# Kernel optimization log

Hardware: AMD Instinct MI355X
Metric: run time of the kernel (lower is better)

## Reference

```python
import jax, jax.numpy as jnp
import numpy as np

NUM_RBF = 16; TOP_K = 32; EDGE_F = 128; NODE_F = 128; NUM_POS = 16; MAX_REL = 32
B, L, M = 2, 1024, 25
# atom order: N=0, Ca=1, C=2, O=3, Cb=4; 24 pairs after the (Ca,Ca) D_neighbors term,
# in the exact order of the torch forward's RBF_all list
PAIR_A = jnp.array([0,2,3,4,1,1,1,1,0,0,0,4,4,3,0,2,3,4,2,3,4,2,3,2])
PAIR_B = jnp.array([0,2,3,4,0,2,3,4,2,3,4,2,3,2,1,1,1,1,0,0,0,4,4,3])


def _rbf(D):
    mu = jnp.linspace(2.0, 22.0, NUM_RBF)
    sig = (22.0 - 2.0) / NUM_RBF
    return jnp.exp(-((D[..., None] - mu) / sig) ** 2)


def _ln(x, g, b, eps=1e-5):
    m = x.mean(-1, keepdims=True)
    v = ((x - m) ** 2).mean(-1, keepdims=True)
    return (x - m) * jax.lax.rsqrt(v + eps) * g + b


def _normalize(v):
    n = jnp.linalg.norm(v, axis=-1, keepdims=True)
    return v / jnp.maximum(n, 1e-12)


def setup_inputs():
    key = jax.random.key(0)
    ks = jax.random.split(key, 16)
    def w(i, shape, scale):
        return jax.random.normal(ks[i], shape, jnp.float32) * scale
    ar = jnp.arange(120, dtype=jnp.int32)
    return {
        "X": w(0, (B, L, 4, 3), 3.0),
        "Y": w(1, (B, L, M, 3), 3.0),
        "Y_m": jnp.ones((B, L, M), jnp.float32),
        "Y_t": jax.random.randint(ks[2], (B, L, M), 0, 120, jnp.int32),
        "mask": jnp.ones((B, L), jnp.float32),
        "R_idx": jnp.tile(jnp.arange(L, dtype=jnp.int32), (B, 1)),
        "chain_labels": jnp.zeros((B, L), jnp.int32),
        # learned params; torch Linear y = x @ W.T + b stored here as [in,out]
        "pos_W": w(3, (2 * MAX_REL + 2, NUM_POS), 0.1),
        "pos_b": jnp.zeros((NUM_POS,), jnp.float32),
        "edge_W": w(4, (NUM_POS + 25 * NUM_RBF, EDGE_F), 0.05),
        "ln_e_g": jnp.ones((EDGE_F,), jnp.float32), "ln_e_b": jnp.zeros((EDGE_F,), jnp.float32),
        "npd_W": w(5, (5 * NUM_RBF + 64 + 4, NODE_F), 0.08),
        "npd_b": jnp.zeros((NODE_F,), jnp.float32),
        "ln_n_g": jnp.ones((NODE_F,), jnp.float32), "ln_n_b": jnp.zeros((NODE_F,), jnp.float32),
        "type_W": w(6, (147, 64), 0.08), "type_b": jnp.zeros((64,), jnp.float32),
        "yn_W": w(7, (147, NODE_F), 0.08),
        "ye_W": w(8, (NUM_RBF, NODE_F), 0.2),
        "ln_ye_g": jnp.ones((NODE_F,), jnp.float32), "ln_ye_b": jnp.zeros((NODE_F,), jnp.float32),
        "ln_yn_g": jnp.ones((NODE_F,), jnp.float32), "ln_yn_b": jnp.zeros((NODE_F,), jnp.float32),
        # periodic table: [atomic_number, group(<19), period(<8)] per element id
        "ptable": jnp.stack([ar, ar % 19, ar % 8]),
    }


def reference(X, Y, Y_m, Y_t, mask, R_idx, chain_labels, pos_W, pos_b, edge_W,
              ln_e_g, ln_e_b, npd_W, npd_b, ln_n_g, ln_n_b, type_W, type_b,
              yn_W, ye_W, ln_ye_g, ln_ye_b, ln_yn_g, ln_yn_b, ptable):
    N, Ca, C, O = X[:, :, 0], X[:, :, 1], X[:, :, 2], X[:, :, 3]
    b = Ca - N; c = C - Ca
    a = jnp.cross(b, c)
    Cb = -0.58273431 * a + 0.56802827 * b - 0.54067466 * c + Ca

    # masked Ca-Ca distances + kNN (smallest)
    m2 = mask[:, :, None] * mask[:, None, :]
    D = m2 * jnp.sqrt(((Ca[:, :, None, :] - Ca[:, None, :, :]) ** 2).sum(-1) + 1e-6)
    D_adjust = D + (1.0 - m2) * D.max(-1, keepdims=True)
    k = min(TOP_K, L)
    neg_D, E_idx = jax.lax.top_k(-D_adjust, k)
    D_neighbors = -neg_D  # [B,L,k]

    atoms = jnp.stack([N, Ca, C, O, Cb])  # [5,B,L,3]
    def pair_rbf(ai, bi):
        A = atoms[ai]; Bc = atoms[bi]
        Dab = jnp.sqrt(((A[:, :, None, :] - Bc[:, None, :, :]) ** 2).sum(-1) + 1e-6)
        return _rbf(jnp.take_along_axis(Dab, E_idx, axis=2))  # [B,L,k,16]
    rbf_pairs = jax.vmap(pair_rbf)(PAIR_A, PAIR_B)  # [24,B,L,k,16]
    RBF_all = jnp.concatenate([_rbf(D_neighbors)[:, :, :, None, :],
                               jnp.moveaxis(rbf_pairs, 0, 3)], axis=3)
    RBF_all = RBF_all.reshape(RBF_all.shape[0], RBF_all.shape[1], k, 25 * NUM_RBF)

    # positional encodings over gathered neighbor offsets
    offset = jnp.take_along_axis(R_idx[:, :, None] - R_idx[:, None, :], E_idx, axis=2)
    d_chains = (chain_labels[:, :, None] == chain_labels[:, None, :]).astype(jnp.int32)
    E_chains = jnp.take_along_axis(d_chains, E_idx, axis=2)
    d = jnp.clip(offset + MAX_REL, 0, 2 * MAX_REL) * E_chains + (1 - E_chains) * (2 * MAX_REL + 1)
    E_pos = jax.nn.one_hot(d, 2 * MAX_REL + 2, dtype=jnp.float32) @ pos_W + pos_b

    E = jnp.concatenate([E_pos, RBF_all], -1) @ edge_W
    E = _ln(E, ln_e_g, ln_e_b)

    # ligand atom type features
    Y_t_1hot_ = jnp.concatenate([
        jax.nn.one_hot(Y_t, 120, dtype=jnp.float32),
        jax.nn.one_hot(ptable[1][Y_t], 19, dtype=jnp.float32),
        jax.nn.one_hot(ptable[2][Y_t], 8, dtype=jnp.float32)], -1)  # [B,L,M,147]
    Y_t_1hot = Y_t_1hot_ @ type_W + type_b  # [B,L,M,64]

    def rbf_to_Y(A):
        return _rbf(jnp.sqrt(((A[:, :, None, :] - Y) ** 2).sum(-1) + 1e-6))
    D_Y = jnp.concatenate([rbf_to_Y(A) for A in (N, Ca, C, O, Cb)], -1)  # [B,L,M,80]

    # local-frame angle features (A=N, B=Ca, C=C)
    e1 = _normalize(N - Ca)
    v2 = C - Ca
    e2 = _normalize(v2 - e1 * (e1 * v2).sum(-1, keepdims=True))
    e3 = jnp.cross(e1, e2)
    R_res = jnp.stack([e1, e2, e3], axis=-1)  # [B,L,3,3], columns e1,e2,e3
    local = jnp.einsum('blqp,blyq->blyp', R_res, Y - Ca[:, :, None, :])
    rxy = jnp.sqrt(local[..., 0] ** 2 + local[..., 1] ** 2 + 1e-8)
    rxyz = jnp.linalg.norm(local, axis=-1) + 1e-8
    f_angles = jnp.stack([local[..., 0] / rxy, local[..., 1] / rxy,
                          rxy / rxyz, local[..., 2] / rxyz], -1)  # [B,L,M,4]

    V = jnp.concatenate([D_Y, Y_t_1hot, f_angles], -1) @ npd_W + npd_b
    V = _ln(V, ln_n_g, ln_n_b)

    Y_edges = _rbf(jnp.sqrt(((Y[:, :, :, None, :] - Y[:, :, None, :, :]) ** 2).sum(-1) + 1e-6)) @ ye_W
    Y_edges = _ln(Y_edges, ln_ye_g, ln_ye_b)
    Y_nodes = _ln(Y_t_1hot_ @ yn_W, ln_yn_g, ln_yn_b)
    return V, E, E_idx, Y_nodes, Y_edges, Y_m
```

## Files before the change

kernel.cpp:

```cpp
#include <hip/hip_runtime.h>
#include <hip/hip_bf16.h>
#include <stdint.h>

#define BB 2
#define LLEN 1024
#define MM 25
#define KK 32

#define OFF_V   0
#define OFF_E   6553600
#define OFF_EI  14942208
#define OFF_YN  15007744
#define OFF_YE  21561344
#define OFF_YM  185401344

#define KP 424
#define KP2 168
#define NR 5

#define NB_YE  (BB*LLEN)
#define NB_E   (BB*LLEN/2)
#define NB_N   ((BB*LLEN+NR-1)/NR)
#define NB_YN  (BB*LLEN*MM/4)
#define VB_E   NB_YE
#define VB_N   (VB_E + NB_E)
#define VB_YN  (VB_N + NB_N)
#define VB_END (VB_YN + NB_YN)

#define SCRATCH_BYTES (680*1024)

typedef __attribute__((ext_vector_type(8))) short short8_t;
typedef __attribute__((ext_vector_type(4))) float f32x4;

__constant__ int g_PA[24] = {0,2,3,4,1,1,1,1,0,0,0,4,4,3,0,2,3,4,2,3,4,2,3,2};
__constant__ int g_PB[24] = {0,2,3,4,0,2,3,4,2,3,4,2,3,2,1,1,1,1,0,0,0,4,4,3};

__device__ __forceinline__ float rbf_val(float d, int r) {
    float mu = 2.0f + (20.0f / 15.0f) * (float)r;
    float z = (d - mu) * 0.8f;
    return __expf(-z * z);
}

__global__ __launch_bounds__(256) void k_pretopk(
    const float* __restrict__ X, const float* __restrict__ mask,
    const float* __restrict__ W, const float* __restrict__ yeW,
    const float* __restrict__ npdW,
    __hip_bfloat16* __restrict__ Bp, __hip_bfloat16* __restrict__ Bp2,
    __hip_bfloat16* __restrict__ Bp3,
    int* __restrict__ eidx, float* __restrict__ dnb,
    float* __restrict__ outEI)
{
    __shared__ float sx[1024], syy[1024], sz[1024], sm[1024];
    int tid = threadIdx.x;

    if (blockIdx.x >= 512) {
        int idx = (blockIdx.x - 512) * 256 + tid;
        if (idx < 6656) {
            int lane = idx & 63, tt = (idx >> 6) & 7, ks = idx >> 9;
            int k0 = ks*32 + (lane >> 4)*8;
            int n  = tt*16 + (lane & 15);
            __hip_bfloat16* dst = Bp + (size_t)idx * 8;
            #pragma unroll
            for (int j = 0; j < 8; ++j) dst[j] = __float2bfloat16(W[(size_t)(k0 + j)*128 + n]);
        } else if (idx < 7168) {
            int i2 = idx - 6656;
            int lane = i2 & 63, tt = i2 >> 6;
            int kg = lane >> 4;
            int n  = tt*16 + (lane & 15);
            __hip_bfloat16* dst = Bp2 + (size_t)i2 * 8;
            #pragma unroll
            for (int j = 0; j < 8; ++j) {
                float v = (kg < 2) ? yeW[(size_t)(kg*8 + j)*128 + n] : 0.0f;
                dst[j] = __float2bfloat16(v);
            }
        } else if (idx < 9728) {
            int i3 = idx - 7168;
            int lane = i3 & 63, tt = (i3 >> 6) & 7, ks = i3 >> 9;
            int k0 = ks*32 + (lane >> 4)*8;
            int n  = tt*16 + (lane & 15);
            __hip_bfloat16* dst = Bp3 + (size_t)i3 * 8;
            #pragma unroll
            for (int j = 0; j < 8; ++j) {
                int k = k0 + j;
                float v = (k < 148) ? npdW[(size_t)k*128 + n] : 0.0f;
                dst[j] = __float2bfloat16(v);
            }
        }
        return;
    }

    int wid = tid >> 6, lane = tid & 63;
    int row0 = blockIdx.x * 4;
    int b = row0 >> 10;
    const float* Xb = X + (size_t)b * LLEN * 12;
    const float* mb = mask + b * LLEN;
    for (int j = tid; j < 1024; j += 256) {
        sx[j]  = Xb[j*12+3];
        syy[j] = Xb[j*12+4];
        sz[j]  = Xb[j*12+5];
        sm[j]  = mb[j];
    }
    __syncthreads();

    int row = row0 + wid, i = row & 1023;
    float cax = sx[i], cay = syy[i], caz = sz[i];
    float mi = sm[i];

    float df[16], mm_[16];
    float lmax = 0.0f;
    #pragma unroll
    for (int q = 0; q < 16; ++q) {
        int j = q*64 + lane;
        float dx = cax - sx[j];
        float dy = cay - syy[j];
        float dz = caz - sz[j];
        float m2 = mi * sm[j];
        float d = sqrtf(dx*dx + dy*dy + dz*dz + 1e-6f) * m2;
        df[q] = d; mm_[q] = m2;
        lmax = fmaxf(lmax, d);
    }
    #pragma unroll
    for (int o = 32; o > 0; o >>= 1) lmax = fmaxf(lmax, __shfl_xor(lmax, o));

    unsigned long long pack[16];
    #pragma unroll
    for (int q = 0; q < 16; ++q) {
        float da = df[q] + (1.0f - mm_[q]) * lmax;
        pack[q] = ((unsigned long long)__float_as_uint(da) << 32) | (unsigned)(q*64 + lane);
    }

    int   myJw = 0;
    float myDv = 0.0f;
    for (int it = 0; it < KK; ++it) {
        unsigned long long lmin = pack[0];
        #pragma unroll
        for (int q = 1; q < 16; ++q) if (pack[q] < lmin) lmin = pack[q];
        #pragma unroll
        for (int o = 32; o > 0; o >>= 1) {
            unsigned long long other = __shfl_xor(lmin, o);
            if (other < lmin) lmin = other;
        }
        int jw = (int)(lmin & 0xffffffffu);
        if (lane == it) { myJw = jw; myDv = __uint_as_float((unsigned)(lmin >> 32)); }
        int lw = jw & 63, qw = jw >> 6;
        #pragma unroll
        for (int q = 0; q < 16; ++q)
            if (lane == lw && q == qw) pack[q] = ~0ull;
    }
    if (lane < KK) {
        eidx[row*KK + lane]  = myJw;
        dnb [row*KK + lane]  = myDv;
        outEI[row*KK + lane] = (float)myJw;
    }
}

union SMem {
    struct { __hip_bfloat16 A[64*KP]; float aj[64][16]; float ai[2][16]; int didx[64]; } e;
    struct { __hip_bfloat16 A[128*KP2]; float sat[NR][15]; float sfr[NR][9]; } n;
    struct { float sy4[32][4]; float stage[4][16*132]; } y;
};

__global__ __launch_bounds__(256) void k_main(
    int vbase,
    const float* __restrict__ X, const float* __restrict__ Y,
    const int* __restrict__ Ridx, const int* __restrict__ chain,
    const float* __restrict__ posW, const float* __restrict__ posb,
    const __hip_bfloat16* __restrict__ Bpack,
    const float* __restrict__ lnEg, const float* __restrict__ lnEb,
    const int* __restrict__ eidx, const float* __restrict__ dnb,
    const int* __restrict__ Yt,
    const float* __restrict__ typeW, const float* __restrict__ typeb,
    const int* __restrict__ ptab,
    const __hip_bfloat16* __restrict__ Bpack3, const float* __restrict__ npdb,
    const float* __restrict__ lnNg, const float* __restrict__ lnNb,
    const __hip_bfloat16* __restrict__ Bpack2,
    const float* __restrict__ lnYEg, const float* __restrict__ lnYEb,
    const float* __restrict__ Ym, const float* __restrict__ ynW,
    const float* __restrict__ lnYNg, const float* __restrict__ lnYNb,
    float* __restrict__ outV, float* __restrict__ outE,
    float* __restrict__ outYN, float* __restrict__ outYE,
    float* __restrict__ outYM)
{
    __shared__ __align__(16) SMem sm;
    int vb = blockIdx.x + vbase;
    int tid = threadIdx.x;
    int wv = tid >> 6, lane = tid & 63;
    int col16 = lane & 15, kg = lane >> 4;

    if (vb >= VB_YN) {
        int row = (vb - VB_YN) * 4 + wv;
        int t = Yt[row];
        int p1 = ptab[120 + t], p2 = ptab[240 + t];
        int r0 = t, r1 = 120 + p1, r2 = 139 + p2;
        float x0 = ynW[r0*128 + lane] + ynW[r1*128 + lane] + ynW[r2*128 + lane];
        float x1 = ynW[r0*128 + 64 + lane] + ynW[r1*128 + 64 + lane] + ynW[r2*128 + 64 + lane];
        float s = x0 + x1, s2 = x0*x0 + x1*x1;
        #pragma unroll
        for (int o = 1; o < 64; o <<= 1) { s += __shfl_xor(s, o); s2 += __shfl_xor(s2, o); }
        float mean = s * (1.0f/128.0f);
        float var  = s2 * (1.0f/128.0f) - mean*mean;
        float inv  = rsqrtf(var + 1e-5f);
        size_t base = (size_t)row * 128;
        outYN[base + lane]      = (x0 - mean)*inv*lnYNg[lane]    + lnYNb[lane];
        outYN[base + 64 + lane] = (x1 - mean)*inv*lnYNg[64+lane] + lnYNb[64+lane];
        if (lane == 0) outYM[row] = Ym[row];
        return;
    }

    if (vb < NB_YE) {
        int row = vb;
        if (tid < 32) { sm.y.sy4[tid][0]=0.f; sm.y.sy4[tid][1]=0.f; sm.y.sy4[tid][2]=0.f; sm.y.sy4[tid][3]=0.f; }
        __syncthreads();
        if (tid < MM*3) ((float*)sm.y.sy4)[ (tid/3)*4 + (tid%3) ] = Y[(size_t)row * MM * 3 + tid];

        short8_t bfr[8];
        const short8_t* B2 = (const short8_t*)Bpack2;
        #pragma unroll
        for (int t = 0; t < 8; ++t) bfr[t] = B2[t*64 + lane];
        float g[8], be[8];
        #pragma unroll
        for (int t = 0; t < 8; ++t) { g[t] = lnYEg[t*16 + col16]; be[t] = lnYEb[t*16 + col16]; }
        __syncthreads();

        float* outR = outYE + (size_t)row * 625 * 128;
        float* sbuf = sm.y.stage[wv];
        for (int T = wv; T < 40; T += 4) {
            int p0 = T * 16;
            int p  = p0 + col16;
            int pc = p < 624 ? p : 624;
            int m1 = pc / 25, m2 = pc - 25*m1;
            float dx = sm.y.sy4[m1][0] - sm.y.sy4[m2][0];
            float dy = sm.y.sy4[m1][1] - sm.y.sy4[m2][1];
            float dz = sm.y.sy4[m1][2] - sm.y.sy4[m2][2];
            float d = sqrtf(dx*dx + dy*dy + dz*dz + 1e-6f);
            union { short8_t v; __hip_bfloat16 h[8]; } ua;
            if (kg < 2) {
                #pragma unroll
                for (int j = 0; j < 8; ++j) ua.h[j] = __float2bfloat16(rbf_val(d, kg*8 + j));
            } else {
                ua.v = (short8_t){0,0,0,0,0,0,0,0};
            }
            f32x4 acc[8];
            #pragma unroll
            for (int t = 0; t < 8; ++t)
                acc[t] = __builtin_amdgcn_mfma_f32_16x16x32_bf16(ua.v, bfr[t],
                             (f32x4){0.f,0.f,0.f,0.f}, 0, 0, 0);
            #pragma unroll
            for (int r = 0; r < 4; ++r) {
                float s = 0.0f;
                #pragma unroll
                for (int t = 0; t < 8; ++t) s += acc[t][r];
                s += __shfl_xor(s, 1); s += __shfl_xor(s, 2);
                s += __shfl_xor(s, 4); s += __shfl_xor(s, 8);
                float mean = s * (1.0f/128.0f);
                float q2 = 0.0f;
                #pragma unroll
                for (int t = 0; t < 8; ++t) { float c0 = acc[t][r] - mean; q2 += c0*c0; }
                q2 += __shfl_xor(q2, 1); q2 += __shfl_xor(q2, 2);
                q2 += __shfl_xor(q2, 4); q2 += __shfl_xor(q2, 8);
                float inv = rsqrtf(q2 * (1.0f/128.0f) + 1e-5f);
                float* sr = sbuf + (kg*4 + r) * 132;
                #pragma unroll
                for (int t = 0; t < 8; ++t) sr[t*16 + col16] = (acc[t][r] - mean)*inv*g[t] + be[t];
            }
            #pragma unroll
            for (int it = 0; it < 8; ++it) {
                int off = it*256 + lane*4;
                int rr = (off >> 7), cc = off & 127;
                float4 v = *(const float4*)(sbuf + rr*132 + cc);
                int gbase = p0*128 + off;
                if (gbase < 80000) *(float4*)(outR + gbase) = v;
            }
        }
        return;
    }

    if (vb < VB_N) {
        int r0 = (vb - VB_E) * 2;
        int b  = r0 >> 10;
        const float* Xb = X + (size_t)b * LLEN * 12;

        if (tid < 64) {
            int e = tid, row = r0 + (e >> 5), k = e & 31;
            int j = eidx[row*KK + k];
            const float* xr = Xb + j*12;
            float nx=xr[0], ny=xr[1], nz=xr[2];
            float ax=xr[3], ay=xr[4], az=xr[5];
            float cx=xr[6], cy=xr[7], cz=xr[8];
            float bx=ax-nx, by=ay-ny, bz=az-nz;
            float vx=cx-ax, vy=cy-ay, vz=cz-az;
            float qx = by*vz - bz*vy, qy = bz*vx - bx*vz, qz = bx*vy - by*vx;
            sm.e.aj[e][0]=nx; sm.e.aj[e][1]=ny; sm.e.aj[e][2]=nz;
            sm.e.aj[e][3]=ax; sm.e.aj[e][4]=ay; sm.e.aj[e][5]=az;
            sm.e.aj[e][6]=cx; sm.e.aj[e][7]=cy; sm.e.aj[e][8]=cz;
            sm.e.aj[e][9]=xr[9]; sm.e.aj[e][10]=xr[10]; sm.e.aj[e][11]=xr[11];
            sm.e.aj[e][12] = -0.58273431f*qx + 0.56802827f*bx - 0.54067466f*vx + ax;
            sm.e.aj[e][13] = -0.58273431f*qy + 0.56802827f*by - 0.54067466f*vy + ay;
            sm.e.aj[e][14] = -0.58273431f*qz + 0.56802827f*bz - 0.54067466f*vz + az;
            int off = Ridx[row] - Ridx[b*LLEN + j];
            int ec = (chain[row] == chain[b*LLEN + j]) ? 1 : 0;
            int dc = off + 32; dc = dc < 0 ? 0 : (dc > 64 ? 64 : dc);
            sm.e.didx[e] = ec ? dc : 65;
        }
        if (tid >= 64 && tid < 66) {
            int rl = tid - 64;
            int i = (r0 + rl) & 1023;
            const float* xr = Xb + i*12;
            float nx=xr[0], ny=xr[1], nz=xr[2];
            float ax=xr[3], ay=xr[4], az=xr[5];
            float cx=xr[6], cy=xr[7], cz=xr[8];
            float bx=ax-nx, by=ay-ny, bz=az-nz;
            float vx=cx-ax, vy=cy-ay, vz=cz-az;
            float qx = by*vz - bz*vy, qy = bz*vx - bx*vz, qz = bx*vy - by*vx;
            sm.e.ai[rl][0]=nx; sm.e.ai[rl][1]=ny; sm.e.ai[rl][2]=nz;
            sm.e.ai[rl][3]=ax; sm.e.ai[rl][4]=ay; sm.e.ai[rl][5]=az;
            sm.e.ai[rl][6]=cx; sm.e.ai[rl][7]=cy; sm.e.ai[rl][8]=cz;
            sm.e.ai[rl][9]=xr[9]; sm.e.ai[rl][10]=xr[10]; sm.e.ai[rl][11]=xr[11];
            sm.e.ai[rl][12] = -0.58273431f*qx + 0.56802827f*bx - 0.54067466f*vx + ax;
            sm.e.ai[rl][13] = -0.58273431f*qy + 0.56802827f*by - 0.54067466f*vy + ay;
            sm.e.ai[rl][14] = -0.58273431f*qz + 0.56802827f*bz - 0.54067466f*vz + az;
        }
        __syncthreads();

        for (int item = tid; item < 64 * 26; item += 256) {
            int e = item / 26, it = item - e * 26;
            int rl = e >> 5;
            union { short8_t v[2]; __hip_bfloat16 h[16]; } uf;
            if (it == 0) {
                int d = sm.e.didx[e];
                #pragma unroll
                for (int c = 0; c < 16; ++c) uf.h[c] = __float2bfloat16(posW[d*16 + c] + posb[c]);
            } else {
                float dist;
                if (it == 1) {
                    dist = dnb[(r0 + rl)*KK + (e & 31)];
                } else {
                    int p = it - 2;
                    int a = g_PA[p], q = g_PB[p];
                    float dx = sm.e.ai[rl][a*3+0] - sm.e.aj[e][q*3+0];
                    float dy = sm.e.ai[rl][a*3+1] - sm.e.aj[e][q*3+1];
                    float dz = sm.e.ai[rl][a*3+2] - sm.e.aj[e][q*3+2];
                    dist = sqrtf(dx*dx + dy*dy + dz*dz + 1e-6f);
                }
                #pragma unroll
                for (int r = 0; r < 16; ++r) uf.h[r] = __float2bfloat16(rbf_val(dist, r));
            }
            short8_t* dst = (short8_t*)(sm.e.A + e * KP + it * 16);
            dst[0] = uf.v[0];
            dst[1] = uf.v[1];
        }
        __syncthreads();

        int wid = tid >> 6;
        f32x4 acc[8];
        #pragma unroll
        for (int t = 0; t < 8; ++t) acc[t] = (f32x4){0.f, 0.f, 0.f, 0.f};
        const __hip_bfloat16* Ar = sm.e.A + (wid*16 + col16) * KP + kg * 8;
        const short8_t* Bp = (const short8_t*)Bpack;
        for (int ks = 0; ks < 13; ++ks) {
            short8_t a = *(const short8_t*)(Ar + ks*32);
            #pragma unroll
            for (int t = 0; t < 8; ++t) {
                short8_t bf = Bp[(ks*8 + t)*64 + lane];
                acc[t] = __builtin_amdgcn_mfma_f32_16x16x32_bf16(a, bf, acc[t], 0, 0, 0);
            }
        }
        __syncthreads();

        float* sbuf = (float*)sm.e.A + wid * (16*132);
        float g[8], be[8];
        #pragma unroll
        for (int t = 0; t < 8; ++t) { g[t] = lnEg[t*16 + col16]; be[t] = lnEb[t*16 + col16]; }
        #pragma unroll
        for (int r = 0; r < 4; ++r) {
            float s = 0.0f;
            #pragma unroll
            for (int t = 0; t < 8; ++t) s += acc[t][r];
            s += __shfl_xor(s, 1); s += __shfl_xor(s, 2);
            s += __shfl_xor(s, 4); s += __shfl_xor(s, 8);
            float mean = s * (1.0f/128.0f);
            float q2 = 0.0f;
            #pragma unroll
            for (int t = 0; t < 8; ++t) { float c0 = acc[t][r] - mean; q2 += c0*c0; }
            q2 += __shfl_xor(q2, 1); q2 += __shfl_xor(q2, 2);
            q2 += __shfl_xor(q2, 4); q2 += __shfl_xor(q2, 8);
            float inv = rsqrtf(q2 * (1.0f/128.0f) + 1e-5f);
            float* sr = sbuf + (kg*4 + r) * 132;
            #pragma unroll
            for (int t = 0; t < 8; ++t) sr[t*16 + col16] = (acc[t][r] - mean)*inv*g[t] + be[t];
        }
        float* gdst = outE + ((size_t)r0 * KK + wid*16) * 128;
        #pragma unroll
        for (int it = 0; it < 8; ++it) {
            int off = it*256 + lane*4;
            int rr = off >> 7, cc = off & 127;
            float4 v = *(const float4*)(sbuf + rr*132 + cc);
            *(float4*)(gdst + off) = v;
        }
        return;
    }

    {
        int r0 = (vb - VB_N) * NR;
        int nrows = (2048 - r0) < NR ? (2048 - r0) : NR;
        int natoms = nrows * MM;

        if (tid < nrows) {
            int row = r0 + tid;
            int b = row >> 10, i = row & 1023;
            const float* xr = X + ((size_t)b * LLEN + i) * 12;
            float nx=xr[0], ny=xr[1], nz=xr[2];
            float ax=xr[3], ay=xr[4], az=xr[5];
            float cx=xr[6], cy=xr[7], cz=xr[8];
            float bx=ax-nx, by=ay-ny, bz=az-nz;
            float vx=cx-ax, vy=cy-ay, vz=cz-az;
            float qx = by*vz - bz*vy, qy = bz*vx - bx*vz, qz = bx*vy - by*vx;
            sm.n.sat[tid][0]=nx; sm.n.sat[tid][1]=ny; sm.n.sat[tid][2]=nz;
            sm.n.sat[tid][3]=ax; sm.n.sat[tid][4]=ay; sm.n.sat[tid][5]=az;
            sm.n.sat[tid][6]=cx; sm.n.sat[tid][7]=cy; sm.n.sat[tid][8]=cz;
            sm.n.sat[tid][9]=xr[9]; sm.n.sat[tid][10]=xr[10]; sm.n.sat[tid][11]=xr[11];
            sm.n.sat[tid][12] = -0.58273431f*qx + 0.56802827f*bx - 0.54067466f*vx + ax;
            sm.n.sat[tid][13] = -0.58273431f*qy + 0.56802827f*by - 0.54067466f*vy + ay;
            sm.n.sat[tid][14] = -0.58273431f*qz + 0.56802827f*bz - 0.54067466f*vz + az;
            float e1x = nx-ax, e1y = ny-ay, e1z = nz-az;
            float n1 = fmaxf(sqrtf(e1x*e1x+e1y*e1y+e1z*e1z), 1e-12f);
            e1x/=n1; e1y/=n1; e1z/=n1;
            float dd = e1x*vx + e1y*vy + e1z*vz;
            float u2x = vx - e1x*dd, u2y = vy - e1y*dd, u2z = vz - e1z*dd;
            float n2 = fmaxf(sqrtf(u2x*u2x+u2y*u2y+u2z*u2z), 1e-12f);
            u2x/=n2; u2y/=n2; u2z/=n2;
            sm.n.sfr[tid][0]=e1x; sm.n.sfr[tid][1]=e1y; sm.n.sfr[tid][2]=e1z;
            sm.n.sfr[tid][3]=u2x; sm.n.sfr[tid][4]=u2y; sm.n.sfr[tid][5]=u2z;
            sm.n.sfr[tid][6]=e1y*u2z - e1z*u2y;
            sm.n.sfr[tid][7]=e1z*u2x - e1x*u2z;
            sm.n.sfr[tid][8]=e1x*u2y - e1y*u2x;
        }
        __syncthreads();

        for (int item = tid; item < natoms * 10; item += 256) {
            int a = item / 10, it = item - a * 10;
            int rl = a / MM, m = a - rl * MM;
            int row = r0 + rl;
            const float* Yb = Y + (size_t)row * MM * 3 + m * 3;
            union { short8_t v[2]; __hip_bfloat16 h[16]; } uf;
            if (it < 5) {
                float dx = sm.n.sat[rl][it*3+0] - Yb[0];
                float dy = sm.n.sat[rl][it*3+1] - Yb[1];
                float dz = sm.n.sat[rl][it*3+2] - Yb[2];
                float dist = sqrtf(dx*dx + dy*dy + dz*dz + 1e-6f);
                #pragma unroll
                for (int r = 0; r < 16; ++r) uf.h[r] = __float2bfloat16(rbf_val(dist, r));
            } else if (it < 9) {
                int qq = it - 5;
                int t = Yt[row*MM + m];
                int p1 = ptab[120 + t], p2 = ptab[240 + t];
                #pragma unroll
                for (int c = 0; c < 16; ++c) {
                    int cc = qq*16 + c;
                    uf.h[c] = __float2bfloat16(typeW[t*64 + cc] + typeW[(120+p1)*64 + cc]
                            + typeW[(139+p2)*64 + cc] + typeb[cc]);
                }
            } else {
                float vx = Yb[0] - sm.n.sat[rl][3];
                float vy = Yb[1] - sm.n.sat[rl][4];
                float vz = Yb[2] - sm.n.sat[rl][5];
                float l0 = sm.n.sfr[rl][0]*vx + sm.n.sfr[rl][1]*vy + sm.n.sfr[rl][2]*vz;
                float l1 = sm.n.sfr[rl][3]*vx + sm.n.sfr[rl][4]*vy + sm.n.sfr[rl][5]*vz;
                float l2 = sm.n.sfr[rl][6]*vx + sm.n.sfr[rl][7]*vy + sm.n.sfr[rl][8]*vz;
                float rxy  = sqrtf(l0*l0 + l1*l1 + 1e-8f);
                float rxyz = sqrtf(l0*l0 + l1*l1 + l2*l2) + 1e-8f;
                uf.h[0] = __float2bfloat16(l0 / rxy);
                uf.h[1] = __float2bfloat16(l1 / rxy);
                uf.h[2] = __float2bfloat16(rxy / rxyz);
                uf.h[3] = __float2bfloat16(l2 / rxyz);
                #pragma unroll
                for (int c = 4; c < 16; ++c) uf.h[c] = __float2bfloat16(0.0f);
            }
            short8_t* dst = (short8_t*)(sm.n.A + a * KP2 + it * 16);
            dst[0] = uf.v[0];
            dst[1] = uf.v[1];
        }
        __syncthreads();

        int wid = tid >> 6;
        const short8_t* Bp = (const short8_t*)Bpack3;
        float g[8], be[8], bias[8];
        #pragma unroll
        for (int t = 0; t < 8; ++t) {
            g[t] = lnNg[t*16 + col16]; be[t] = lnNb[t*16 + col16];
            bias[t] = npdb[t*16 + col16];
        }
        #pragma unroll
        for (int half = 0; half < 2; ++half) {
            int tile = wid + half*4;
            int abase = tile * 16;
            if (abase < natoms) {
                const __hip_bfloat16* Ar = sm.n.A + (abase + col16) * KP2 + kg * 8;
                f32x4 acc[8];
                #pragma unroll
                for (int t = 0; t < 8; ++t) acc[t] = (f32x4){0.f, 0.f, 0.f, 0.f};
                for (int ks = 0; ks < 5; ++ks) {
                    short8_t a = *(const short8_t*)(Ar + ks*32);
                    #pragma unroll
                    for (int t = 0; t < 8; ++t) {
                        short8_t bf = Bp[(ks*8 + t)*64 + lane];
                        acc[t] = __builtin_amdgcn_mfma_f32_16x16x32_bf16(a, bf, acc[t], 0, 0, 0);
                    }
                }
                #pragma unroll
                for (int r = 0; r < 4; ++r) {
                    float s = 0.0f;
                    #pragma unroll
                    for (int t = 0; t < 8; ++t) { acc[t][r] += bias[t]; s += acc[t][r]; }
                    s += __shfl_xor(s, 1); s += __shfl_xor(s, 2);
                    s += __shfl_xor(s, 4); s += __shfl_xor(s, 8);
                    float mean = s * (1.0f/128.0f);
                    float q2 = 0.0f;
                    #pragma unroll
                    for (int t = 0; t < 8; ++t) { float c0 = acc[t][r] - mean; q2 += c0*c0; }
                    q2 += __shfl_xor(q2, 1); q2 += __shfl_xor(q2, 2);
                    q2 += __shfl_xor(q2, 4); q2 += __shfl_xor(q2, 8);
                    float inv = rsqrtf(q2 * (1.0f/128.0f) + 1e-5f);
                    int aa = abase + kg*4 + r;
                    if (aa < natoms) {
                        float* dst = outV + ((size_t)r0 * MM + aa) * 128 + col16;
                        #pragma unroll
                        for (int t = 0; t < 8; ++t) dst[t*16] = (acc[t][r] - mean)*inv*g[t] + be[t];
                    }
                }
            }
        }
    }
}

extern "C" void kernel_launch(void* const* d_in, const int* in_sizes, int n_in,
                              void* d_out, int out_size, void* d_ws, size_t ws_size,
                              hipStream_t stream) {
    const float* X     = (const float*)d_in[0];
    const float* Y     = (const float*)d_in[1];
    const float* Ym    = (const float*)d_in[2];
    const int*   Yt    = (const int*)d_in[3];
    const float* mask  = (const float*)d_in[4];
    const int*   Ridx  = (const int*)d_in[5];
    const int*   chain = (const int*)d_in[6];
    const float* posW  = (const float*)d_in[7];
    const float* posb  = (const float*)d_in[8];
    const float* edgeW = (const float*)d_in[9];
    const float* lnEg  = (const float*)d_in[10];
    const float* lnEb  = (const float*)d_in[11];
    const float* npdW  = (const float*)d_in[12];
    const float* npdb  = (const float*)d_in[13];
    const float* lnNg  = (const float*)d_in[14];
    const float* lnNb  = (const float*)d_in[15];
    const float* typeW = (const float*)d_in[16];
    const float* typeb = (const float*)d_in[17];
    const float* ynW   = (const float*)d_in[18];
    const float* yeW   = (const float*)d_in[19];
    const float* lnYEg = (const float*)d_in[20];
    const float* lnYEb = (const float*)d_in[21];
    const float* lnYNg = (const float*)d_in[22];
    const float* lnYNb = (const float*)d_in[23];
    const int*   ptab  = (const int*)d_in[24];

    float* o = (float*)d_out;
    bool ws_ok = (ws_size >= (size_t)SCRATCH_BYTES);
    char* scratch = ws_ok ? (char*)d_ws : (char*)(o + OFF_YN);
    int*   eidx = (int*)scratch;
    float* dnb  = (float*)(scratch + BB*LLEN*KK*4);
    __hip_bfloat16* Bpack  = (__hip_bfloat16*)(scratch + 2*BB*LLEN*KK*4);
    __hip_bfloat16* Bpack2 = Bpack + 6656*8;
    __hip_bfloat16* Bpack3 = Bpack2 + 512*8;

    k_pretopk<<<550, 256, 0, stream>>>(X, mask, edgeW, yeW, npdW,
                                       Bpack, Bpack2, Bpack3,
                                       eidx, dnb, o + OFF_EI);
    if (ws_ok) {
        k_main<<<VB_END, 256, 0, stream>>>(0,
            X, Y, Ridx, chain, posW, posb, Bpack, lnEg, lnEb, eidx, dnb,
            Yt, typeW, typeb, ptab, Bpack3, npdb, lnNg, lnNb,
            Bpack2, lnYEg, lnYEb, Ym, ynW, lnYNg, lnYNb,
            o + OFF_V, o + OFF_E, o + OFF_YN, o + OFF_YE, o + OFF_YM);
    } else {
        k_main<<<VB_YN, 256, 0, stream>>>(0,
            X, Y, Ridx, chain, posW, posb, Bpack, lnEg, lnEb, eidx, dnb,
            Yt, typeW, typeb, ptab, Bpack3, npdb, lnNg, lnNb,
            Bpack2, lnYEg, lnYEb, Ym, ynW, lnYNg, lnYNb,
            o + OFF_V, o + OFF_E, o + OFF_YN, o + OFF_YE, o + OFF_YM);
        k_main<<<NB_YN, 256, 0, stream>>>(VB_YN,
            X, Y, Ridx, chain, posW, posb, Bpack, lnEg, lnEb, eidx, dnb,
            Yt, typeW, typeb, ptab, Bpack3, npdb, lnNg, lnNb,
            Bpack2, lnYEg, lnYEb, Ym, ynW, lnYNg, lnYNb,
            o + OFF_V, o + OFF_E, o + OFF_YN, o + OFF_YE, o + OFF_YM);
    }
}
```

Before: 239.8 us.

## Move Y_nodes layernorm blocks from main kernel into the top-k prep kernel

Moves the Y_nodes embedding-sum plus layernorm work (12800 small blocks) out of the heavy main kernel and into the first kernel, next to the top-k and weight-packing blocks. The main kernel then carries fewer blocks and a smaller argument set, and the light Y_nodes work can fill the GPU while the top-k blocks run. The first kernel uses 16KB of shared memory, so the added blocks may see lower occupancy than they had in the main kernel. The fallback path reorders its launches so Y_nodes still runs after the scratch region is no longer needed.

```diff
diff --git a/kernel.cpp b/kernel.cpp
--- a/kernel.cpp
+++ b/kernel.cpp
@@ -18,14 +18,13 @@
 #define KP2 168
 #define NR 5
 
+#define P1_PREP 512
+#define P1_YN   550
+#define P1_END  (P1_YN + BB*LLEN*MM/4)
 #define NB_YE  (BB*LLEN)
-#define NB_E   (BB*LLEN/2)
-#define NB_N   ((BB*LLEN+NR-1)/NR)
-#define NB_YN  (BB*LLEN*MM/4)
 #define VB_E   NB_YE
-#define VB_N   (VB_E + NB_E)
-#define VB_YN  (VB_N + NB_N)
-#define VB_END (VB_YN + NB_YN)
+#define VB_N   (VB_E + BB*LLEN/2)
+#define VB_END (VB_N + (BB*LLEN+NR-1)/NR)
 
 #define SCRATCH_BYTES (680*1024)
 
@@ -41,32 +40,59 @@
     return __expf(-z * z);
 }
 
-__global__ __launch_bounds__(256) void k_pretopk(
+__global__ __launch_bounds__(256) void k_phase1(
+    int vbase,
     const float* __restrict__ X, const float* __restrict__ mask,
     const float* __restrict__ W, const float* __restrict__ yeW,
     const float* __restrict__ npdW,
     __hip_bfloat16* __restrict__ Bp, __hip_bfloat16* __restrict__ Bp2,
     __hip_bfloat16* __restrict__ Bp3,
     int* __restrict__ eidx, float* __restrict__ dnb,
-    float* __restrict__ outEI)
+    float* __restrict__ outEI,
+    const int* __restrict__ Yt, const float* __restrict__ Ym,
+    const int* __restrict__ ptab, const float* __restrict__ ynW,
+    const float* __restrict__ lnYNg, const float* __restrict__ lnYNb,
+    float* __restrict__ outYN, float* __restrict__ outYM)
 {
-    __shared__ float sx[1024], syy[1024], sz[1024], sm[1024];
+    __shared__ float sx[1024], syy[1024], sz[1024], smk[1024];
+    int vb = blockIdx.x + vbase;
     int tid = threadIdx.x;
-
-    if (blockIdx.x >= 512) {
-        int idx = (blockIdx.x - 512) * 256 + tid;
+    int wid = tid >> 6, lane = tid & 63;
+
+    if (vb >= P1_YN) {
+        int row = (vb - P1_YN) * 4 + wid;
+        int t = Yt[row];
+        int p1 = ptab[120 + t], p2 = ptab[240 + t];
+        int r0 = t, r1 = 120 + p1, r2 = 139 + p2;
+        float x0 = ynW[r0*128 + lane] + ynW[r1*128 + lane] + ynW[r2*128 + lane];
+        float x1 = ynW[r0*128 + 64 + lane] + ynW[r1*128 + 64 + lane] + ynW[r2*128 + 64 + lane];
+        float s = x0 + x1, s2 = x0*x0 + x1*x1;
+        #pragma unroll
+        for (int o = 1; o < 64; o <<= 1) { s += __shfl_xor(s, o); s2 += __shfl_xor(s2, o); }
+        float mean = s * (1.0f/128.0f);
+        float var  = s2 * (1.0f/128.0f) - mean*mean;
+        float inv  = rsqrtf(var + 1e-5f);
+        size_t base = (size_t)row * 128;
+        outYN[base + lane]      = (x0 - mean)*inv*lnYNg[lane]    + lnYNb[lane];
+        outYN[base + 64 + lane] = (x1 - mean)*inv*lnYNg[64+lane] + lnYNb[64+lane];
+        if (lane == 0) outYM[row] = Ym[row];
+        return;
+    }
+
+    if (vb >= P1_PREP) {
+        int idx = (vb - P1_PREP) * 256 + tid;
         if (idx < 6656) {
-            int lane = idx & 63, tt = (idx >> 6) & 7, ks = idx >> 9;
-            int k0 = ks*32 + (lane >> 4)*8;
-            int n  = tt*16 + (lane & 15);
+            int ln = idx & 63, tt = (idx >> 6) & 7, ks = idx >> 9;
+            int k0 = ks*32 + (ln >> 4)*8;
+            int n  = tt*16 + (ln & 15);
             __hip_bfloat16* dst = Bp + (size_t)idx * 8;
             #pragma unroll
             for (int j = 0; j < 8; ++j) dst[j] = __float2bfloat16(W[(size_t)(k0 + j)*128 + n]);
         } else if (idx < 7168) {
             int i2 = idx - 6656;
-            int lane = i2 & 63, tt = i2 >> 6;
-            int kg = lane >> 4;
-            int n  = tt*16 + (lane & 15);
+            int ln = i2 & 63, tt = i2 >> 6;
+            int kg = ln >> 4;
+            int n  = tt*16 + (ln & 15);
             __hip_bfloat16* dst = Bp2 + (size_t)i2 * 8;
             #pragma unroll
             for (int j = 0; j < 8; ++j) {
@@ -75,9 +101,9 @@
             }
         } else if (idx < 9728) {
             int i3 = idx - 7168;
-            int lane = i3 & 63, tt = (i3 >> 6) & 7, ks = i3 >> 9;
-            int k0 = ks*32 + (lane >> 4)*8;
-            int n  = tt*16 + (lane & 15);
+            int ln = i3 & 63, tt = (i3 >> 6) & 7, ks = i3 >> 9;
+            int k0 = ks*32 + (ln >> 4)*8;
+            int n  = tt*16 + (ln & 15);
             __hip_bfloat16* dst = Bp3 + (size_t)i3 * 8;
             #pragma unroll
             for (int j = 0; j < 8; ++j) {
@@ -89,8 +115,7 @@
         return;
     }
 
-    int wid = tid >> 6, lane = tid & 63;
-    int row0 = blockIdx.x * 4;
+    int row0 = vb * 4;
     int b = row0 >> 10;
     const float* Xb = X + (size_t)b * LLEN * 12;
     const float* mb = mask + b * LLEN;
@@ -98,13 +123,13 @@
         sx[j]  = Xb[j*12+3];
         syy[j] = Xb[j*12+4];
         sz[j]  = Xb[j*12+5];
-        sm[j]  = mb[j];
+        smk[j] = mb[j];
     }
     __syncthreads();
 
     int row = row0 + wid, i = row & 1023;
     float cax = sx[i], cay = syy[i], caz = sz[i];
-    float mi = sm[i];
+    float mi = smk[i];
 
     float df[16], mm_[16];
     float lmax = 0.0f;
@@ -114,7 +139,7 @@
         float dx = cax - sx[j];
         float dy = cay - syy[j];
         float dz = caz - sz[j];
-        float m2 = mi * sm[j];
+        float m2 = mi * smk[j];
         float d = sqrtf(dx*dx + dy*dy + dz*dz + 1e-6f) * m2;
         df[q] = d; mm_[q] = m2;
         lmax = fmaxf(lmax, d);
@@ -160,8 +185,7 @@
     struct { float sy4[32][4]; float stage[4][16*132]; } y;
 };
 
-__global__ __launch_bounds__(256) void k_main(
-    int vbase,
+__global__ __launch_bounds__(256) void k_phase2(
     const float* __restrict__ X, const float* __restrict__ Y,
     const int* __restrict__ Ridx, const int* __restrict__ chain,
     const float* __restrict__ posW, const float* __restrict__ posb,
@@ -175,37 +199,14 @@
     const float* __restrict__ lnNg, const float* __restrict__ lnNb,
     const __hip_bfloat16* __restrict__ Bpack2,
     const float* __restrict__ lnYEg, const float* __restrict__ lnYEb,
-    const float* __restrict__ Ym, const float* __restrict__ ynW,
-    const float* __restrict__ lnYNg, const float* __restrict__ lnYNb,
     float* __restrict__ outV, float* __restrict__ outE,
-    float* __restrict__ outYN, float* __restrict__ outYE,
-    float* __restrict__ outYM)
+    float* __restrict__ outYE)
 {
     __shared__ __align__(16) SMem sm;
-    int vb = blockIdx.x + vbase;
+    int vb = blockIdx.x;
     int tid = threadIdx.x;
     int wv = tid >> 6, lane = tid & 63;
     int col16 = lane & 15, kg = lane >> 4;
-
-    if (vb >= VB_YN) {
-        int row = (vb - VB_YN) * 4 + wv;
-        int t = Yt[row];
-        int p1 = ptab[120 + t], p2 = ptab[240 + t];
-        int r0 = t, r1 = 120 + p1, r2 = 139 + p2;
-        float x0 = ynW[r0*128 + lane] + ynW[r1*128 + lane] + ynW[r2*128 + lane];
-        float x1 = ynW[r0*128 + 64 + lane] + ynW[r1*128 + 64 + lane] + ynW[r2*128 + 64 + lane];
-        float s = x0 + x1, s2 = x0*x0 + x1*x1;
-        #pragma unroll
-        for (int o = 1; o < 64; o <<= 1) { s += __shfl_xor(s, o); s2 += __shfl_xor(s2, o); }
-        float mean = s * (1.0f/128.0f);
-        float var  = s2 * (1.0f/128.0f) - mean*mean;
-        float inv  = rsqrtf(var + 1e-5f);
-        size_t base = (size_t)row * 128;
-        outYN[base + lane]      = (x0 - mean)*inv*lnYNg[lane]    + lnYNb[lane];
-        outYN[base + 64 + lane] = (x1 - mean)*inv*lnYNg[64+lane] + lnYNb[64+lane];
-        if (lane == 0) outYM[row] = Ym[row];
-        return;
-    }
 
     if (vb < NB_YE) {
         int row = vb;
@@ -571,25 +572,24 @@
     __hip_bfloat16* Bpack2 = Bpack + 6656*8;
     __hip_bfloat16* Bpack3 = Bpack2 + 512*8;
 
-    k_pretopk<<<550, 256, 0, stream>>>(X, mask, edgeW, yeW, npdW,
-                                       Bpack, Bpack2, Bpack3,
-                                       eidx, dnb, o + OFF_EI);
     if (ws_ok) {
-        k_main<<<VB_END, 256, 0, stream>>>(0,
+        k_phase1<<<P1_END, 256, 0, stream>>>(0, X, mask, edgeW, yeW, npdW,
+            Bpack, Bpack2, Bpack3, eidx, dnb, o + OFF_EI,
+            Yt, Ym, ptab, ynW, lnYNg, lnYNb, o + OFF_YN, o + OFF_YM);
+        k_phase2<<<VB_END, 256, 0, stream>>>(
             X, Y, Ridx, chain, posW, posb, Bpack, lnEg, lnEb, eidx, dnb,
             Yt, typeW, typeb, ptab, Bpack3, npdb, lnNg, lnNb,
-            Bpack2, lnYEg, lnYEb, Ym, ynW, lnYNg, lnYNb,
-            o + OFF_V, o + OFF_E, o + OFF_YN, o + OFF_YE, o + OFF_YM);
+            Bpack2, lnYEg, lnYEb, o + OFF_V, o + OFF_E, o + OFF_YE);
     } else {
-        k_main<<<VB_YN, 256, 0, stream>>>(0,
+        k_phase1<<<P1_YN, 256, 0, stream>>>(0, X, mask, edgeW, yeW, npdW,
+            Bpack, Bpack2, Bpack3, eidx, dnb, o + OFF_EI,
+            Yt, Ym, ptab, ynW, lnYNg, lnYNb, o + OFF_YN, o + OFF_YM);
+        k_phase2<<<VB_END, 256, 0, stream>>>(
             X, Y, Ridx, chain, posW, posb, Bpack, lnEg, lnEb, eidx, dnb,
             Yt, typeW, typeb, ptab, Bpack3, npdb, lnNg, lnNb,
-            Bpack2, lnYEg, lnYEb, Ym, ynW, lnYNg, lnYNb,
-            o + OFF_V, o + OFF_E, o + OFF_YN, o + OFF_YE, o + OFF_YM);
-        k_main<<<NB_YN, 256, 0, stream>>>(VB_YN,
-            X, Y, Ridx, chain, posW, posb, Bpack, lnEg, lnEb, eidx, dnb,
-            Yt, typeW, typeb, ptab, Bpack3, npdb, lnNg, lnNb,
-            Bpack2, lnYEg, lnYEb, Ym, ynW, lnYNg, lnYNb,
-            o + OFF_V, o + OFF_E, o + OFF_YN, o + OFF_YE, o + OFF_YM);
+            Bpack2, lnYEg, lnYEb, o + OFF_V, o + OFF_E, o + OFF_YE);
+        k_phase1<<<P1_END - P1_YN, 256, 0, stream>>>(P1_YN, X, mask, edgeW, yeW, npdW,
+            Bpack, Bpack2, Bpack3, eidx, dnb, o + OFF_EI,
+            Yt, Ym, ptab, ynW, lnYNg, lnYNb, o + OFF_YN, o + OFF_YM);
     }
 }
```

Result: faster. 218.8 us (-8.8%).
